# Kernel tuning notes

Hardware: AMD Instinct MI355X
Metric: run time of the kernel (lower is better)

## Reference

```python
import jax, jax.numpy as jnp
import numpy as np

N, E, F, H, C = 50000, 800000, 100, 128, 40
EPS = 1e-5


def setup_inputs() -> dict:
    key = jax.random.key(0)
    ks = jax.random.split(key, 9)
    s = 0.05
    return {
        "x": jax.random.normal(ks[0], (N, F), jnp.float32),
        "nbr": jax.random.normal(ks[1], (E, F), jnp.float32),
        "seg_ids": jnp.sort(jax.random.randint(ks[2], (E,), 0, N)),
        "W1x": jax.random.normal(ks[3], (H, F), jnp.float32) * s,
        "W1n": jax.random.normal(ks[4], (H, F), jnp.float32) * s,
        "g1": jnp.ones((), jnp.float32),
        "b1": jnp.zeros((), jnp.float32),
        "W2x": jax.random.normal(ks[5], (H, H), jnp.float32) * s,
        "W2n": jax.random.normal(ks[6], (H, H), jnp.float32) * s,
        "g2": jnp.ones((), jnp.float32),
        "b2": jnp.zeros((), jnp.float32),
        "Wc": jax.random.normal(ks[7], (C, H), jnp.float32) * s,
        "bc": jnp.zeros((C,), jnp.float32),
    }


def _seg_mean(v, ids, n):
    # ragged per-node neighbor mean: segment_sum / count
    s = jax.ops.segment_sum(v, ids, num_segments=n)
    cnt = jax.ops.segment_sum(jnp.ones((v.shape[0],), v.dtype), ids, num_segments=n)
    return s / jnp.maximum(cnt, 1.0)[:, None], cnt


def _bn_relu(t, g, b):
    # BatchNorm1d(1) in training mode on [N,1,d]: scalar mean/var over all elements
    m = t.mean()
    v = jnp.mean((t - m) ** 2)
    return jax.nn.relu(g * (t - m) * jax.lax.rsqrt(v + EPS) + b)


def _seg_bn_relu(nbr, ids, cnt, g, b, n):
    # BN applied per neighbor-list tensor: scalar stats per segment (over k_i * d elems)
    d = nbr.shape[1]
    ne = jnp.maximum(cnt * d, 1.0)
    sm = jax.ops.segment_sum(nbr.sum(axis=1), ids, num_segments=n) / ne
    sq = jax.ops.segment_sum((nbr * nbr).sum(axis=1), ids, num_segments=n) / ne
    var = sq - sm * sm
    inv = jax.lax.rsqrt(var + EPS)
    xn = (nbr - sm[ids, None]) * inv[ids, None]
    return jax.nn.relu(g * xn + b)


def reference(x, nbr, seg_ids, W1x, W1n, g1, b1, W2x, W2n, g2, b2, Wc, bc):
    n = x.shape[0]
    # layer 1: FeatTrans(feat_len -> hidden)
    f, cnt = _seg_mean(nbr, seg_ids, n)          # [N,F]
    h = x @ W1x.T + f @ W1n.T                    # [N,H]
    nbr1 = nbr @ W1x.T                           # [E,H]
    # acvt1
    h = _bn_relu(h, g1, b1)
    nbr1 = _seg_bn_relu(nbr1, seg_ids, cnt, g1, b1, n)
    # layer 2: FeatTrans(hidden -> hidden)
    f2, _ = _seg_mean(nbr1, seg_ids, n)          # [N,H]
    h = h @ W2x.T + f2 @ W2n.T                   # [N,H]
    # acvt2 + classifier
    h = _bn_relu(h, g2, b2)
    return h @ Wc.T + bc                         # [N,C]
```

## Files before the change

### kernel.cpp

```cpp
#include <hip/hip_runtime.h>
#include <hip/hip_bf16.h>
#include <math.h>

#define NN 50000
#define NE 800000
#define FD 100
#define HD 128
#define CD 40
#define EPSF 1e-5f
#define NTILE 6250
#define GRID_EDGE 256
#define NT_NODE 391

typedef __attribute__((ext_vector_type(8))) short short8;
typedef __attribute__((ext_vector_type(4))) float f32x4;

__device__ __forceinline__ unsigned short f2bf(float x) {
  union { __hip_bfloat16 h; unsigned short u; } cv;
  cv.h = __float2bfloat16(x);
  return cv.u;
}
__device__ __forceinline__ float bf2f(unsigned short b) {
  return __uint_as_float(((unsigned)b) << 16);
}

__device__ __forceinline__ void bar_lds() {
  asm volatile("s_waitcnt lgkmcnt(0)\n\ts_barrier" ::: "memory");
}

__global__ void k_rowptr(const int* __restrict__ seg, int* __restrict__ rp) {
  int i = blockIdx.x * blockDim.x + threadIdx.x;
  if (i > NN) return;
  int lo = 0, hi = NE;
  while (lo < hi) { int mid = (lo + hi) >> 1; if (seg[mid] < i) lo = mid + 1; else hi = mid; }
  rp[i] = lo;
}

__device__ __forceinline__ void cvt_write256(const float4* gv, char* rowbase, int q, int sr) {
  const float* vf = (const float*)gv;
#pragma unroll
  for (int h = 0; h < 4; ++h) {
    short8 s;
#pragma unroll
    for (int e = 0; e < 8; ++e) s[e] = (short)f2bf(vf[h * 8 + e]);
    *(short8*)(rowbase + ((q * 64 + h * 16) ^ ((sr & 7) << 4))) = s;
  }
}

__device__ __forceinline__ void load_quarters(const float* src, int q, float4* gv) {
#pragma unroll
  for (int i4 = 0; i4 < 8; ++i4) {
    const int c = q * 32 + i4 * 4;
    gv[i4] = (c < FD) ? *(const float4*)(src + c) : make_float4(0.f, 0.f, 0.f, 0.f);
  }
}

__global__ __launch_bounds__(512, 2) void k_gemm1(
    const float* __restrict__ nbr, const int* __restrict__ seg,
    const float* __restrict__ W1x,
    float* __restrict__ es, float* __restrict__ eq, float* __restrict__ fsum) {
  __shared__ char lds[98304];
  __shared__ int segL[2][128];
  const int tid = threadIdx.x;
  const int sr = tid >> 2, q = tid & 3;
  const int w = tid >> 6, l = tid & 63, lr = l & 15, lh = l >> 4;

  {
    float4 gv[8];
    load_quarters(W1x + (size_t)sr * FD, q, gv);
    cvt_write256(gv, lds + sr * 256, q, sr);
  }
  {
    float4 gv[8];
    load_quarters(nbr + (size_t)(blockIdx.x * 128 + sr) * FD, q, gv);
    if (tid < 128) segL[0][tid] = seg[blockIdx.x * 128 + tid];
    __syncthreads();
    cvt_write256(gv, lds + 32768 + sr * 256, q, sr);
  }
  int cur = 0;
  for (int t = blockIdx.x; t < NTILE; t += GRID_EDGE) {
    const int tn = t + GRID_EDGE;
    float4 gv[8];
    int sgn = 0;
    if (tn < NTILE) {
      load_quarters(nbr + (size_t)(tn * 128 + sr) * FD, q, gv);
      if (tid < 128) sgn = seg[tn * 128 + tid];
    }
    bar_lds();
    const char* bufc = lds + 32768 + cur * 32768;
    short8 af[4];
    const int arow = w * 16 + lr;
#pragma unroll
    for (int kk = 0; kk < 4; ++kk)
      af[kk] = *(const short8*)(bufc + arow * 256 + ((lh * 16 + kk * 64) ^ ((arow & 7) << 4)));

    const size_t rowb = (size_t)t * 128;
    float rs[4] = {0.f, 0.f, 0.f, 0.f}, rq[4] = {0.f, 0.f, 0.f, 0.f};
#pragma unroll
    for (int nt = 0; nt < 8; ++nt) {
      f32x4 acc = {0.f, 0.f, 0.f, 0.f};
#pragma unroll
      for (int kk = 0; kk < 4; ++kk) {
        const int n = nt * 16 + lr;
        const short8 bfg = *(const short8*)(lds + n * 256 + ((lh * 16 + kk * 64) ^ ((n & 7) << 4)));
        acc = __builtin_amdgcn_mfma_f32_16x16x32_bf16(af[kk], bfg, acc, 0, 0, 0);
      }
#pragma unroll
      for (int r = 0; r < 4; ++r) {
        const float val = acc[r];
        rs[r] += val;
        rq[r] = fmaf(val, val, rq[r]);
      }
    }
#pragma unroll
    for (int r = 0; r < 4; ++r) {
      float a = rs[r], b = rq[r];
#pragma unroll
      for (int off = 1; off < 16; off <<= 1) { a += __shfl_xor(a, off); b += __shfl_xor(b, off); }
      if (lr == 0) {
        const size_t rg = rowb + w * 16 + lh * 4 + r;
        es[rg] = a; eq[rg] = b;
      }
    }
    {
      const int qq = tid >> 7, j = tid & 127;
      if (j < FD) {
        const int r0 = qq * 32;
        const int* sl = segL[cur];
        int curn = sl[r0];
        float acc = 0.f;
        bool inside = false;
#pragma unroll
        for (int b8 = 0; b8 < 4; ++b8) {
          float vals[8];
#pragma unroll
          for (int k = 0; k < 8; ++k) {
            const int row = r0 + b8 * 8 + k;
            vals[k] = bf2f(*(const unsigned short*)(bufc + row * 256 + ((j * 2) ^ ((row & 7) << 4))));
          }
#pragma unroll
          for (int k = 0; k < 8; ++k) {
            const int nd = sl[r0 + b8 * 8 + k];
            if (nd != curn) {
              float* dst = fsum + (size_t)curn * FD + j;
              if (inside) *dst = acc; else atomicAdd(dst, acc);
              inside = true; acc = 0.f; curn = nd;
            }
            acc += vals[k];
          }
        }
        atomicAdd(fsum + (size_t)curn * FD + j, acc);
      }
    }
    if (tn < NTILE) {
      cvt_write256(gv, lds + 32768 + (cur ^ 1) * 32768 + sr * 256, q, sr);
      if (tid < 128) segL[cur ^ 1][tid] = sgn;
    }
    cur ^= 1;
  }
}

__global__ void k_nodestats(const int* __restrict__ rp, const float* __restrict__ es,
                            const float* __restrict__ eq, float2* __restrict__ smi,
                            float* __restrict__ rcv) {
  const int i = blockIdx.x * blockDim.x + threadIdx.x;
  if (i >= NN) return;
  const int s = rp[i], e = rp[i + 1];
  float S = 0.f, Q = 0.f;
  for (int ed = s; ed < e; ++ed) { S += es[ed]; Q += eq[ed]; }
  const int cnt = e - s;
  const float ne = fmaxf((float)cnt * (float)HD, 1.f);
  const float sm = S / ne;
  const float var = Q / ne - sm * sm;
  smi[i] = make_float2(sm, rsqrtf(var + EPSF));
  rcv[i] = 1.f / (float)(cnt > 0 ? cnt : 1);
}

__global__ __launch_bounds__(512, 2) void k_fuse2(
    const float* __restrict__ nbr, const int* __restrict__ seg,
    const float* __restrict__ W1x, const float2* __restrict__ smi,
    const float* __restrict__ g1p, const float* __restrict__ b1p,
    float* __restrict__ f2sum) {
  __shared__ char lds[98304];
  __shared__ int segL[2][128];
  __shared__ float2 smrow[2][128];
  const int tid = threadIdx.x;
  const int sr = tid >> 2, q = tid & 3;
  const int w = tid >> 6, l = tid & 63, lr = l & 15, lh = l >> 4;
  const float g1 = g1p[0], b1 = b1p[0];
  char* A = lds + 32768;
  char* P = lds + 65536;

  {
    float4 gv[8];
    load_quarters(W1x + (size_t)sr * FD, q, gv);
    cvt_write256(gv, lds + sr * 256, q, sr);
  }
  {
    float4 gv[8];
    load_quarters(nbr + (size_t)(blockIdx.x * 128 + sr) * FD, q, gv);
    if (tid < 128) {
      const int nd = seg[blockIdx.x * 128 + tid];
      segL[0][tid] = nd;
      smrow[0][tid] = smi[nd];
    }
    __syncthreads();
    cvt_write256(gv, A + sr * 256, q, sr);
  }
  int cur = 0;
  for (int t = blockIdx.x; t < NTILE; t += GRID_EDGE) {
    const int tn = t + GRID_EDGE;
    float4 gv[8];
    int sgn = 0;
    float2 smn = make_float2(0.f, 0.f);
    if (tn < NTILE) {
      load_quarters(nbr + (size_t)(tn * 128 + sr) * FD, q, gv);
      if (tid < 128) { sgn = seg[tn * 128 + tid]; smn = smi[sgn]; }
    }
    bar_lds();
    short8 af[4];
    const int arow = w * 16 + lr;
#pragma unroll
    for (int kk = 0; kk < 4; ++kk)
      af[kk] = *(const short8*)(A + arow * 256 + ((lh * 16 + kk * 64) ^ ((arow & 7) << 4)));
    float2 mi[4];
#pragma unroll
    for (int r = 0; r < 4; ++r) mi[r] = smrow[cur][w * 16 + lh * 4 + r];
#pragma unroll
    for (int nt = 0; nt < 8; ++nt) {
      f32x4 acc = {0.f, 0.f, 0.f, 0.f};
#pragma unroll
      for (int kk = 0; kk < 4; ++kk) {
        const int n = nt * 16 + lr;
        const short8 bfg = *(const short8*)(lds + n * 256 + ((lh * 16 + kk * 64) ^ ((n & 7) << 4)));
        acc = __builtin_amdgcn_mfma_f32_16x16x32_bf16(af[kk], bfg, acc, 0, 0, 0);
      }
      const int col = nt * 16 + lr;
#pragma unroll
      for (int r = 0; r < 4; ++r) {
        const int row = w * 16 + lh * 4 + r;
        const float v = fmaxf(fmaf(g1, (acc[r] - mi[r].x) * mi[r].y, b1), 0.f);
        *(unsigned short*)(P + row * 256 + ((col * 2) ^ ((row & 7) << 4))) = f2bf(v);
      }
    }
    bar_lds();
    {
      const int qq = tid >> 7, j = tid & 127;
      const int r0 = qq * 32;
      const int* sl = segL[cur];
      int curn = sl[r0];
      float acc = 0.f;
      bool inside = false;
#pragma unroll
      for (int b8 = 0; b8 < 4; ++b8) {
        float vals[8];
#pragma unroll
        for (int k = 0; k < 8; ++k) {
          const int row = r0 + b8 * 8 + k;
          vals[k] = bf2f(*(const unsigned short*)(P + row * 256 + ((j * 2) ^ ((row & 7) << 4))));
        }
#pragma unroll
        for (int k = 0; k < 8; ++k) {
          const int nd = sl[r0 + b8 * 8 + k];
          if (nd != curn) {
            float* dst = f2sum + (size_t)curn * HD + j;
            if (inside) *dst = acc; else atomicAdd(dst, acc);
            inside = true; acc = 0.f; curn = nd;
          }
          acc += vals[k];
        }
      }
      atomicAdd(f2sum + (size_t)curn * HD + j, acc);
    }
    if (tn < NTILE) {
      cvt_write256(gv, A + sr * 256, q, sr);
      if (tid < 128) { segL[cur ^ 1][tid] = sgn; smrow[cur ^ 1][tid] = smn; }
    }
    cur ^= 1;
  }
}

template <bool L2>
__global__ __launch_bounds__(512) void k_ngemm(
    const float* __restrict__ P1, const float* __restrict__ P2,
    const float* __restrict__ rcv,
    const float* __restrict__ WA, const float* __restrict__ WB,
    const float* __restrict__ stats_in,
    const float* __restrict__ gp, const float* __restrict__ bp,
    float* __restrict__ out, float* __restrict__ so) {
  constexpr int KH = L2 ? HD : FD;
  __shared__ char lds[131072];
  __shared__ float sred[16];
  const int tid = threadIdx.x;
  float a1 = 1.f, c1 = 0.f;
  if (L2) {
    const float m = stats_in[0] * (1.f / ((float)NN * (float)HD));
    const float var = stats_in[1] * (1.f / ((float)NN * (float)HD)) - m * m;
    const float inv = rsqrtf(var + EPSF);
    a1 = gp[0] * inv; c1 = bp[0] - gp[0] * m * inv;
  }
  const int sr = tid >> 2, q = tid & 3;
  const bool half2 = (q >= 2);
  const int cbase = (q & 1) * 64;
  {
    const float* src = (half2 ? WB : WA) + (size_t)sr * KH;
    float v[64];
#pragma unroll
    for (int i4 = 0; i4 < 16; ++i4) {
      const int c = cbase + i4 * 4;
      float4 tv = make_float4(0.f, 0.f, 0.f, 0.f);
      if (c < KH) tv = *(const float4*)(src + c);
      v[i4 * 4 + 0] = tv.x; v[i4 * 4 + 1] = tv.y; v[i4 * 4 + 2] = tv.z; v[i4 * 4 + 3] = tv.w;
    }
    char* db = lds + 65536 + sr * 512;
#pragma unroll
    for (int h = 0; h < 8; ++h) {
      short8 s8;
#pragma unroll
      for (int e = 0; e < 8; ++e) s8[e] = (short)f2bf(v[h * 8 + e]);
      *(short8*)(db + ((q * 128 + h * 16) ^ ((sr & 7) << 4))) = s8;
    }
  }
  const int w = tid >> 6, l = tid & 63, lr = l & 15, lh = l >> 4;
  float ls = 0.f, lsq = 0.f;
  for (int bt = blockIdx.x; bt < NT_NODE; bt += gridDim.x) {
    __syncthreads();
    const size_t rg = (size_t)bt * 128 + sr;
    {
      const float* src = (half2 ? P2 : P1) + rg * KH;
      const float sc = half2 ? ((rg < NN) ? rcv[rg] : 0.f) : 1.f;
      float v[64];
#pragma unroll
      for (int i4 = 0; i4 < 16; ++i4) {
        const int c = cbase + i4 * 4;
        float4 tv = make_float4(0.f, 0.f, 0.f, 0.f);
        if (rg < NN && c < KH) tv = *(const float4*)(src + c);
        float e0 = tv.x, e1 = tv.y, e2 = tv.z, e3 = tv.w;
        if (half2) { e0 *= sc; e1 *= sc; e2 *= sc; e3 *= sc; }
        else if (L2 && rg < NN) {
          e0 = fmaxf(fmaf(a1, e0, c1), 0.f); e1 = fmaxf(fmaf(a1, e1, c1), 0.f);
          e2 = fmaxf(fmaf(a1, e2, c1), 0.f); e3 = fmaxf(fmaf(a1, e3, c1), 0.f);
        }
        v[i4 * 4 + 0] = e0; v[i4 * 4 + 1] = e1; v[i4 * 4 + 2] = e2; v[i4 * 4 + 3] = e3;
      }
      char* db = lds + sr * 512;
#pragma unroll
      for (int h = 0; h < 8; ++h) {
        short8 s8;
#pragma unroll
        for (int e = 0; e < 8; ++e) s8[e] = (short)f2bf(v[h * 8 + e]);
        *(short8*)(db + ((q * 128 + h * 16) ^ ((sr & 7) << 4))) = s8;
      }
    }
    __syncthreads();
    short8 af[8];
    const int arow = w * 16 + lr;
#pragma unroll
    for (int kk = 0; kk < 8; ++kk)
      af[kk] = *(const short8*)(lds + arow * 512 + ((lh * 16 + kk * 64) ^ ((arow & 7) << 4)));
    const char* B = lds + 65536;
#pragma unroll
    for (int nt = 0; nt < 8; ++nt) {
      f32x4 acc = {0.f, 0.f, 0.f, 0.f};
#pragma unroll
      for (int kk = 0; kk < 8; ++kk) {
        const int n = nt * 16 + lr;
        const short8 bfg = *(const short8*)(B + n * 512 + ((lh * 16 + kk * 64) ^ ((n & 7) << 4)));
        acc = __builtin_amdgcn_mfma_f32_16x16x32_bf16(af[kk], bfg, acc, 0, 0, 0);
      }
      const int col = nt * 16 + lr;
#pragma unroll
      for (int r = 0; r < 4; ++r) {
        const float val = acc[r];
        const size_t rg2 = (size_t)bt * 128 + w * 16 + lh * 4 + r;
        if (rg2 < NN) out[rg2 * HD + col] = val;
        ls += val;
        lsq = fmaf(val, val, lsq);
      }
    }
  }
#pragma unroll
  for (int off = 32; off > 0; off >>= 1) { ls += __shfl_down(ls, off); lsq += __shfl_down(lsq, off); }
  if ((tid & 63) == 0) { sred[(tid >> 6) * 2] = ls; sred[(tid >> 6) * 2 + 1] = lsq; }
  __syncthreads();
  if (tid == 0) {
    float S = 0.f, Q = 0.f;
#pragma unroll
    for (int i = 0; i < 8; ++i) { S += sred[i * 2]; Q += sred[i * 2 + 1]; }
    atomicAdd(&so[0], S);
    atomicAdd(&so[1], Q);
  }
}

__global__ __launch_bounds__(512) void k_cls(
    const float* __restrict__ h2, const float* __restrict__ Wc,
    const float* __restrict__ bc, const float* __restrict__ stats,
    const float* __restrict__ gp, const float* __restrict__ bp,
    float* __restrict__ out) {
  __shared__ char lds[45056];
  const int tid = threadIdx.x;
  const float m = stats[0] * (1.f / ((float)NN * (float)HD));
  const float var = stats[1] * (1.f / ((float)NN * (float)HD)) - m * m;
  const float inv = rsqrtf(var + EPSF);
  const float g = gp[0], bb = bp[0];
  const float a2 = g * inv, c2 = bb - g * m * inv;
  const int sr = tid >> 2, q = tid & 3;
  const size_t rg = (size_t)blockIdx.x * 128 + sr;
  {
    float4 gv[8];
#pragma unroll
    for (int i4 = 0; i4 < 8; ++i4) {
      const int c = q * 32 + i4 * 4;
      float4 t = (rg < NN) ? *(const float4*)(h2 + rg * HD + c) : make_float4(0.f, 0.f, 0.f, 0.f);
      t.x = fmaxf(fmaf(a2, t.x, c2), 0.f); t.y = fmaxf(fmaf(a2, t.y, c2), 0.f);
      t.z = fmaxf(fmaf(a2, t.z, c2), 0.f); t.w = fmaxf(fmaf(a2, t.w, c2), 0.f);
      gv[i4] = t;
    }
    cvt_write256(gv, lds + sr * 256, q, sr);
  }
  if (tid < 192) {
    const int bn = tid >> 2, bq = tid & 3;
    float4 gv[8];
#pragma unroll
    for (int i4 = 0; i4 < 8; ++i4) {
      const int c = bq * 32 + i4 * 4;
      gv[i4] = (bn < CD) ? *(const float4*)(Wc + (size_t)bn * HD + c) : make_float4(0.f, 0.f, 0.f, 0.f);
    }
    cvt_write256(gv, lds + 32768 + bn * 256, bq, bn);
  }
  __syncthreads();
  const int w = tid >> 6, l = tid & 63, lr = l & 15, lh = l >> 4;
  short8 af[4];
  const int arow = w * 16 + lr;
#pragma unroll
  for (int kk = 0; kk < 4; ++kk)
    af[kk] = *(const short8*)(lds + arow * 256 + ((lh * 16 + kk * 64) ^ ((arow & 7) << 4)));
#pragma unroll
  for (int nt = 0; nt < 3; ++nt) {
    f32x4 acc = {0.f, 0.f, 0.f, 0.f};
#pragma unroll
    for (int kk = 0; kk < 4; ++kk) {
      const int n = nt * 16 + lr;
      const short8 bfg = *(const short8*)(lds + 32768 + n * 256 + ((lh * 16 + kk * 64) ^ ((n & 7) << 4)));
      acc = __builtin_amdgcn_mfma_f32_16x16x32_bf16(af[kk], bfg, acc, 0, 0, 0);
    }
    const int col = nt * 16 + lr;
    if (col < CD) {
      const float bias = bc[col];
#pragma unroll
      for (int r = 0; r < 4; ++r) {
        const size_t rg2 = (size_t)blockIdx.x * 128 + w * 16 + lh * 4 + r;
        if (rg2 < NN) out[rg2 * CD + col] = acc[r] + bias;
      }
    }
  }
}

extern "C" void kernel_launch(void* const* d_in, const int* in_sizes, int n_in,
                              void* d_out, int out_size, void* d_ws, size_t ws_size,
                              hipStream_t stream) {
  const float* x   = (const float*)d_in[0];
  const float* nbr = (const float*)d_in[1];
  const int*   seg = (const int*)d_in[2];
  const float* W1x = (const float*)d_in[3];
  const float* W1n = (const float*)d_in[4];
  const float* g1  = (const float*)d_in[5];
  const float* b1  = (const float*)d_in[6];
  const float* W2x = (const float*)d_in[7];
  const float* W2n = (const float*)d_in[8];
  const float* g2  = (const float*)d_in[9];
  const float* b2  = (const float*)d_in[10];
  const float* Wc  = (const float*)d_in[11];
  const float* bc  = (const float*)d_in[12];
  float* out = (float*)d_out;

  char* p = (char*)d_ws;
  auto alloc = [&](size_t bytes) {
    char* q = p;
    p += (bytes + 255) & ~(size_t)255;
    return q;
  };
  int*    rp    = (int*)   alloc(sizeof(int) * (NN + 1));
  float*  fsum  = (float*) alloc(sizeof(float) * (size_t)NN * FD);
  float*  f2sum = (float*) alloc(sizeof(float) * (size_t)NN * HD);
  float*  hpre  = (float*) alloc(sizeof(float) * (size_t)NN * HD);
  float*  h2    = (float*) alloc(sizeof(float) * (size_t)NN * HD);
  float*  stats = (float*) alloc(sizeof(float) * 4);
  float*  es    = (float*) alloc(sizeof(float) * (size_t)NE);
  float*  eq    = (float*) alloc(sizeof(float) * (size_t)NE);
  float2* smi   = (float2*)alloc(sizeof(float2) * (size_t)NN);
  float*  rcv   = (float*) alloc(sizeof(float) * (size_t)NN);

  hipMemsetAsync(stats, 0, sizeof(float) * 4, stream);
  hipMemsetAsync(fsum, 0, sizeof(float) * (size_t)NN * FD, stream);
  hipMemsetAsync(f2sum, 0, sizeof(float) * (size_t)NN * HD, stream);

  k_rowptr<<<(NN + 256) / 256, 256, 0, stream>>>(seg, rp);
  k_gemm1<<<GRID_EDGE, 512, 0, stream>>>(nbr, seg, W1x, es, eq, fsum);
  k_nodestats<<<(NN + 255) / 256, 256, 0, stream>>>(rp, es, eq, smi, rcv);
  k_fuse2<<<GRID_EDGE, 512, 0, stream>>>(nbr, seg, W1x, smi, g1, b1, f2sum);
  k_ngemm<false><<<256, 512, 0, stream>>>(x, fsum, rcv, W1x, W1n, stats, g1, b1, hpre, stats);
  k_ngemm<true><<<256, 512, 0, stream>>>(hpre, f2sum, rcv, W2x, W2n, stats, g1, b1, h2, stats + 2);
  k_cls<<<NT_NODE, 512, 0, stream>>>(h2, Wc, bc, stats + 2, g2, b2, out);
}
```

Measured before the change: 447.1 us.

## Single-buffer edge kernels to double occupancy and grid; atomically reduce per-node stats

The two edge kernels drop their double-buffered LDS tiles for a single 32 KB tile, with extra barriers. This cuts shared memory per block so launch bounds can ask for 4 blocks per CU, and the edge grid is doubled. k_fuse2 also writes the post-BN activations back into the same A buffer instead of a separate P buffer. k_gemm1 now reduces per-edge sum and sum-of-squares straight into per-node accumulators with atomics, so the per-edge es/eq arrays and the serial per-node loop in k_nodestats go away. In exchange, loads are no longer overlapped by double buffering, each iteration pays extra barriers, and there is more atomic traffic.

```diff
diff --git a/kernel.cpp b/kernel.cpp
--- a/kernel.cpp
+++ b/kernel.cpp
@@ -9,7 +9,7 @@
 #define CD 40
 #define EPSF 1e-5f
 #define NTILE 6250
-#define GRID_EDGE 256
+#define GRID_EDGE 512
 #define NT_NODE 391
 
 typedef __attribute__((ext_vector_type(8))) short short8;
@@ -55,12 +55,13 @@
   }
 }
 
-__global__ __launch_bounds__(512, 2) void k_gemm1(
+__global__ __launch_bounds__(512, 4) void k_gemm1(
     const float* __restrict__ nbr, const int* __restrict__ seg,
     const float* __restrict__ W1x,
-    float* __restrict__ es, float* __restrict__ eq, float* __restrict__ fsum) {
-  __shared__ char lds[98304];
-  __shared__ int segL[2][128];
+    float* __restrict__ Ssum, float* __restrict__ Qsum, float* __restrict__ fsum) {
+  __shared__ char lds[65536];
+  __shared__ int segL[128];
+  char* A = lds + 32768;
   const int tid = threadIdx.x;
   const int sr = tid >> 2, q = tid & 3;
   const int w = tid >> 6, l = tid & 63, lr = l & 15, lh = l >> 4;
@@ -69,15 +70,10 @@
     float4 gv[8];
     load_quarters(W1x + (size_t)sr * FD, q, gv);
     cvt_write256(gv, lds + sr * 256, q, sr);
-  }
-  {
-    float4 gv[8];
     load_quarters(nbr + (size_t)(blockIdx.x * 128 + sr) * FD, q, gv);
-    if (tid < 128) segL[0][tid] = seg[blockIdx.x * 128 + tid];
-    __syncthreads();
-    cvt_write256(gv, lds + 32768 + sr * 256, q, sr);
-  }
-  int cur = 0;
+    cvt_write256(gv, A + sr * 256, q, sr);
+    if (tid < 128) segL[tid] = seg[blockIdx.x * 128 + tid];
+  }
   for (int t = blockIdx.x; t < NTILE; t += GRID_EDGE) {
     const int tn = t + GRID_EDGE;
     float4 gv[8];
@@ -87,14 +83,12 @@
       if (tid < 128) sgn = seg[tn * 128 + tid];
     }
     bar_lds();
-    const char* bufc = lds + 32768 + cur * 32768;
     short8 af[4];
     const int arow = w * 16 + lr;
 #pragma unroll
     for (int kk = 0; kk < 4; ++kk)
-      af[kk] = *(const short8*)(bufc + arow * 256 + ((lh * 16 + kk * 64) ^ ((arow & 7) << 4)));
-
-    const size_t rowb = (size_t)t * 128;
+      af[kk] = *(const short8*)(A + arow * 256 + ((lh * 16 + kk * 64) ^ ((arow & 7) << 4)));
+
     float rs[4] = {0.f, 0.f, 0.f, 0.f}, rq[4] = {0.f, 0.f, 0.f, 0.f};
 #pragma unroll
     for (int nt = 0; nt < 8; ++nt) {
@@ -112,22 +106,32 @@
         rq[r] = fmaf(val, val, rq[r]);
       }
     }
+    float sv[4], qv[4];
 #pragma unroll
     for (int r = 0; r < 4; ++r) {
       float a = rs[r], b = rq[r];
 #pragma unroll
       for (int off = 1; off < 16; off <<= 1) { a += __shfl_xor(a, off); b += __shfl_xor(b, off); }
-      if (lr == 0) {
-        const size_t rg = rowb + w * 16 + lh * 4 + r;
-        es[rg] = a; eq[rg] = b;
-      }
+      sv[r] = a; qv[r] = b;
+    }
+    if (lr == 0) {
+      const int R = w * 16 + lh * 4;
+      const int4 nid = *(const int4*)&segL[R];
+      float sa = sv[0], qa = qv[0];
+      int curn = nid.x;
+      if (nid.y != curn) { atomicAdd(&Ssum[curn], sa); atomicAdd(&Qsum[curn], qa); sa = 0.f; qa = 0.f; curn = nid.y; }
+      sa += sv[1]; qa += qv[1];
+      if (nid.z != curn) { atomicAdd(&Ssum[curn], sa); atomicAdd(&Qsum[curn], qa); sa = 0.f; qa = 0.f; curn = nid.z; }
+      sa += sv[2]; qa += qv[2];
+      if (nid.w != curn) { atomicAdd(&Ssum[curn], sa); atomicAdd(&Qsum[curn], qa); sa = 0.f; qa = 0.f; curn = nid.w; }
+      sa += sv[3]; qa += qv[3];
+      atomicAdd(&Ssum[curn], sa); atomicAdd(&Qsum[curn], qa);
     }
     {
       const int qq = tid >> 7, j = tid & 127;
       if (j < FD) {
         const int r0 = qq * 32;
-        const int* sl = segL[cur];
-        int curn = sl[r0];
+        int curn = segL[r0];
         float acc = 0.f;
         bool inside = false;
 #pragma unroll
@@ -136,11 +140,11 @@
 #pragma unroll
           for (int k = 0; k < 8; ++k) {
             const int row = r0 + b8 * 8 + k;
-            vals[k] = bf2f(*(const unsigned short*)(bufc + row * 256 + ((j * 2) ^ ((row & 7) << 4))));
+            vals[k] = bf2f(*(const unsigned short*)(A + row * 256 + ((j * 2) ^ ((row & 7) << 4))));
           }
 #pragma unroll
           for (int k = 0; k < 8; ++k) {
-            const int nd = sl[r0 + b8 * 8 + k];
+            const int nd = segL[r0 + b8 * 8 + k];
             if (nd != curn) {
               float* dst = fsum + (size_t)curn * FD + j;
               if (inside) *dst = acc; else atomicAdd(dst, acc);
@@ -152,62 +156,53 @@
         atomicAdd(fsum + (size_t)curn * FD + j, acc);
       }
     }
+    bar_lds();
     if (tn < NTILE) {
-      cvt_write256(gv, lds + 32768 + (cur ^ 1) * 32768 + sr * 256, q, sr);
-      if (tid < 128) segL[cur ^ 1][tid] = sgn;
-    }
-    cur ^= 1;
-  }
-}
-
-__global__ void k_nodestats(const int* __restrict__ rp, const float* __restrict__ es,
-                            const float* __restrict__ eq, float2* __restrict__ smi,
+      cvt_write256(gv, A + sr * 256, q, sr);
+      if (tid < 128) segL[tid] = sgn;
+    }
+  }
+}
+
+__global__ void k_nodestats(const int* __restrict__ rp, const float* __restrict__ Ssum,
+                            const float* __restrict__ Qsum, float2* __restrict__ smi,
                             float* __restrict__ rcv) {
   const int i = blockIdx.x * blockDim.x + threadIdx.x;
   if (i >= NN) return;
-  const int s = rp[i], e = rp[i + 1];
-  float S = 0.f, Q = 0.f;
-  for (int ed = s; ed < e; ++ed) { S += es[ed]; Q += eq[ed]; }
-  const int cnt = e - s;
+  const int cnt = rp[i + 1] - rp[i];
   const float ne = fmaxf((float)cnt * (float)HD, 1.f);
-  const float sm = S / ne;
-  const float var = Q / ne - sm * sm;
+  const float sm = Ssum[i] / ne;
+  const float var = Qsum[i] / ne - sm * sm;
   smi[i] = make_float2(sm, rsqrtf(var + EPSF));
   rcv[i] = 1.f / (float)(cnt > 0 ? cnt : 1);
 }
 
-__global__ __launch_bounds__(512, 2) void k_fuse2(
+__global__ __launch_bounds__(512, 4) void k_fuse2(
     const float* __restrict__ nbr, const int* __restrict__ seg,
     const float* __restrict__ W1x, const float2* __restrict__ smi,
     const float* __restrict__ g1p, const float* __restrict__ b1p,
     float* __restrict__ f2sum) {
-  __shared__ char lds[98304];
-  __shared__ int segL[2][128];
-  __shared__ float2 smrow[2][128];
+  __shared__ char lds[65536];
+  __shared__ int segL[128];
+  __shared__ float2 smrow[128];
+  char* A = lds + 32768;
   const int tid = threadIdx.x;
   const int sr = tid >> 2, q = tid & 3;
   const int w = tid >> 6, l = tid & 63, lr = l & 15, lh = l >> 4;
   const float g1 = g1p[0], b1 = b1p[0];
-  char* A = lds + 32768;
-  char* P = lds + 65536;
 
   {
     float4 gv[8];
     load_quarters(W1x + (size_t)sr * FD, q, gv);
     cvt_write256(gv, lds + sr * 256, q, sr);
-  }
-  {
-    float4 gv[8];
     load_quarters(nbr + (size_t)(blockIdx.x * 128 + sr) * FD, q, gv);
+    cvt_write256(gv, A + sr * 256, q, sr);
     if (tid < 128) {
       const int nd = seg[blockIdx.x * 128 + tid];
-      segL[0][tid] = nd;
-      smrow[0][tid] = smi[nd];
-    }
-    __syncthreads();
-    cvt_write256(gv, A + sr * 256, q, sr);
-  }
-  int cur = 0;
+      segL[tid] = nd;
+      smrow[tid] = smi[nd];
+    }
+  }
   for (int t = blockIdx.x; t < NTILE; t += GRID_EDGE) {
     const int tn = t + GRID_EDGE;
     float4 gv[8];
@@ -225,7 +220,8 @@
       af[kk] = *(const short8*)(A + arow * 256 + ((lh * 16 + kk * 64) ^ ((arow & 7) << 4)));
     float2 mi[4];
 #pragma unroll
-    for (int r = 0; r < 4; ++r) mi[r] = smrow[cur][w * 16 + lh * 4 + r];
+    for (int r = 0; r < 4; ++r) mi[r] = smrow[w * 16 + lh * 4 + r];
+    bar_lds();
 #pragma unroll
     for (int nt = 0; nt < 8; ++nt) {
       f32x4 acc = {0.f, 0.f, 0.f, 0.f};
@@ -240,15 +236,14 @@
       for (int r = 0; r < 4; ++r) {
         const int row = w * 16 + lh * 4 + r;
         const float v = fmaxf(fmaf(g1, (acc[r] - mi[r].x) * mi[r].y, b1), 0.f);
-        *(unsigned short*)(P + row * 256 + ((col * 2) ^ ((row & 7) << 4))) = f2bf(v);
+        *(unsigned short*)(A + row * 256 + ((col * 2) ^ ((row & 7) << 4))) = f2bf(v);
       }
     }
     bar_lds();
     {
       const int qq = tid >> 7, j = tid & 127;
       const int r0 = qq * 32;
-      const int* sl = segL[cur];
-      int curn = sl[r0];
+      int curn = segL[r0];
       float acc = 0.f;
       bool inside = false;
 #pragma unroll
@@ -257,11 +252,11 @@
 #pragma unroll
         for (int k = 0; k < 8; ++k) {
           const int row = r0 + b8 * 8 + k;
-          vals[k] = bf2f(*(const unsigned short*)(P + row * 256 + ((j * 2) ^ ((row & 7) << 4))));
+          vals[k] = bf2f(*(const unsigned short*)(A + row * 256 + ((j * 2) ^ ((row & 7) << 4))));
         }
 #pragma unroll
         for (int k = 0; k < 8; ++k) {
-          const int nd = sl[r0 + b8 * 8 + k];
+          const int nd = segL[r0 + b8 * 8 + k];
           if (nd != curn) {
             float* dst = f2sum + (size_t)curn * HD + j;
             if (inside) *dst = acc; else atomicAdd(dst, acc);
@@ -272,11 +267,11 @@
       }
       atomicAdd(f2sum + (size_t)curn * HD + j, acc);
     }
+    bar_lds();
     if (tn < NTILE) {
       cvt_write256(gv, A + sr * 256, q, sr);
-      if (tid < 128) { segL[cur ^ 1][tid] = sgn; smrow[cur ^ 1][tid] = smn; }
-    }
-    cur ^= 1;
+      if (tid < 128) { segL[tid] = sgn; smrow[tid] = smn; }
+    }
   }
 }
 
@@ -486,18 +481,20 @@
   float*  hpre  = (float*) alloc(sizeof(float) * (size_t)NN * HD);
   float*  h2    = (float*) alloc(sizeof(float) * (size_t)NN * HD);
   float*  stats = (float*) alloc(sizeof(float) * 4);
-  float*  es    = (float*) alloc(sizeof(float) * (size_t)NE);
-  float*  eq    = (float*) alloc(sizeof(float) * (size_t)NE);
+  float*  Ssum  = (float*) alloc(sizeof(float) * (size_t)NN);
+  float*  Qsum  = (float*) alloc(sizeof(float) * (size_t)NN);
   float2* smi   = (float2*)alloc(sizeof(float2) * (size_t)NN);
   float*  rcv   = (float*) alloc(sizeof(float) * (size_t)NN);
 
   hipMemsetAsync(stats, 0, sizeof(float) * 4, stream);
   hipMemsetAsync(fsum, 0, sizeof(float) * (size_t)NN * FD, stream);
   hipMemsetAsync(f2sum, 0, sizeof(float) * (size_t)NN * HD, stream);
+  hipMemsetAsync(Ssum, 0, sizeof(float) * (size_t)NN, stream);
+  hipMemsetAsync(Qsum, 0, sizeof(float) * (size_t)NN, stream);
 
   k_rowptr<<<(NN + 256) / 256, 256, 0, stream>>>(seg, rp);
-  k_gemm1<<<GRID_EDGE, 512, 0, stream>>>(nbr, seg, W1x, es, eq, fsum);
-  k_nodestats<<<(NN + 255) / 256, 256, 0, stream>>>(rp, es, eq, smi, rcv);
+  k_gemm1<<<GRID_EDGE, 512, 0, stream>>>(nbr, seg, W1x, Ssum, Qsum, fsum);
+  k_nodestats<<<(NN + 255) / 256, 256, 0, stream>>>(rp, Ssum, Qsum, smi, rcv);
   k_fuse2<<<GRID_EDGE, 512, 0, stream>>>(nbr, seg, W1x, smi, g1, b1, f2sum);
   k_ngemm<false><<<256, 512, 0, stream>>>(x, fsum, rcv, W1x, W1n, stats, g1, b1, hpre, stats);
   k_ngemm<true><<<256, 512, 0, stream>>>(hpre, f2sum, rcv, W2x, W2n, stats, g1, b1, h2, stats + 2);
```

New measurement: 425.9 us. 4.7% less time.
